# Optimization experiments

Hardware: AMD Instinct MI355X
Metric: run time of the kernel (lower is better)

## Reference

```python
import jax, jax.numpy as jnp
import numpy as np

D_MODEL = 1024
NUM_HEADS = 16
D_K = D_MODEL // NUM_HEADS


def setup_inputs() -> dict:
    key = jax.random.key(0)
    ks = jax.random.split(key, 8)
    B, S = 2, 2048
    s = 1.0 / np.sqrt(D_MODEL)
    return {
        "query": jax.random.normal(ks[0], (B, S, D_MODEL), jnp.float32),
        "key": jax.random.normal(ks[1], (B, S, D_MODEL), jnp.float32),
        "value": jax.random.normal(ks[2], (B, S, D_MODEL), jnp.float32),
        "Wq": jax.random.normal(ks[3], (D_MODEL, D_MODEL), jnp.float32) * s,
        "bq": jnp.zeros((D_MODEL,), jnp.float32),
        "Wk": jax.random.normal(ks[4], (D_MODEL, D_MODEL), jnp.float32) * s,
        "bk": jnp.zeros((D_MODEL,), jnp.float32),
        "Wv": jax.random.normal(ks[5], (D_MODEL, D_K), jnp.float32) * s,
        "bv": jnp.zeros((D_K,), jnp.float32),
        "Wo": jax.random.normal(ks[6], (D_K, D_MODEL), jnp.float32) * (1.0 / np.sqrt(D_K)),
        "bo": jnp.zeros((D_MODEL,), jnp.float32),
    }


def reference(query, key, value, Wq, bq, Wk, bk, Wv, bv, Wo, bo):
    B, S, _ = query.shape
    scale = jnp.sqrt(jnp.asarray(D_K, query.dtype))
    # Per-head Q, K: [B, H, S, d_k]
    Q = (query @ Wq + bq).reshape(B, S, NUM_HEADS, D_K).transpose(0, 2, 1, 3)
    K = (key @ Wk + bk).reshape(B, -1, NUM_HEADS, D_K).transpose(0, 2, 1, 3)
    # Shared V across heads: [B, S, d_k]
    V = value @ Wv + bv
    scores = jnp.einsum("bhqd,bhkd->bhqk", Q, K) / scale
    attn = jax.nn.softmax(scores, axis=-1)
    avg_attn = attn.mean(axis=1)            # [B, S, S] head-averaged weights
    attn_output = jnp.einsum("bqk,bkd->bqd", avg_attn, V)
    output = attn_output @ Wo + bo
    return (output, avg_attn)
```

## Files before the change

kernel.cpp:

```cpp
#include <hip/hip_runtime.h>

#define BATCH 2
#define SEQ   2048
#define DMODEL 1024
#define NHEAD 16
#define DK    64
#define MROWS (BATCH * SEQ)
#define KSPLIT 4

using bf16x8 = __attribute__((ext_vector_type(8))) short;
using f32x4  = __attribute__((ext_vector_type(4))) float;

__device__ __forceinline__ unsigned short f2bf_rne(float x) {
    unsigned u = __float_as_uint(x);
    u += 0x7FFFu + ((u >> 16) & 1u);
    return (unsigned short)(u >> 16);
}
__device__ __forceinline__ float bf2f(unsigned short h) {
    return __uint_as_float((unsigned)h << 16);
}

__device__ __forceinline__ long long qf_addr(int row, int d) {
    const int qt = row >> 4, lid = row & 15;
    const int hh = d >> 6, ch = (d >> 3) & 7, j = d & 7;
    return ((((long long)qt * NHEAD + hh) * 8 + ch) * 16 + lid) * 8 + j;
}

__global__ __launch_bounds__(256) void conv_split_kernel(
    const float* __restrict__ x, unsigned short* __restrict__ hi,
    unsigned short* __restrict__ lo)
{
    const long long i = ((long long)blockIdx.x * 256 + threadIdx.x) * 4;
    float4 v = *(const float4*)&x[i];
    ushort4 h4, l4;
    unsigned short h;
    h = f2bf_rne(v.x); h4.x = h; l4.x = f2bf_rne(v.x - bf2f(h));
    h = f2bf_rne(v.y); h4.y = h; l4.y = f2bf_rne(v.y - bf2f(h));
    h = f2bf_rne(v.z); h4.z = h; l4.z = f2bf_rne(v.z - bf2f(h));
    h = f2bf_rne(v.w); h4.w = h; l4.w = f2bf_rne(v.w - bf2f(h));
    *(ushort4*)&hi[i] = h4;
    *(ushort4*)&lo[i] = l4;
}

__global__ __launch_bounds__(256) void conv_splitT_kernel(
    const float* __restrict__ W, unsigned short* __restrict__ hiT,
    unsigned short* __restrict__ loT)
{
    const int k0 = blockIdx.y * 64;
    const int n0 = blockIdx.x * 64;
    const int tid = threadIdx.x;
    __shared__ float T[64][68];
#pragma unroll
    for (int it = 0; it < 4; ++it) {
        const int r = it * 16 + (tid >> 4);
        const int c = (tid & 15) * 4;
        float4 v = *(const float4*)&W[(long long)(k0 + r) * DMODEL + n0 + c];
        T[r][c] = v.x; T[r][c + 1] = v.y; T[r][c + 2] = v.z; T[r][c + 3] = v.w;
    }
    __syncthreads();
#pragma unroll
    for (int it = 0; it < 4; ++it) {
        const int n = it * 16 + (tid >> 4);
        const int kc = (tid & 15) * 4;
        ushort4 h4, l4;
        float v; unsigned short h;
        v = T[kc + 0][n]; h = f2bf_rne(v); h4.x = h; l4.x = f2bf_rne(v - bf2f(h));
        v = T[kc + 1][n]; h = f2bf_rne(v); h4.y = h; l4.y = f2bf_rne(v - bf2f(h));
        v = T[kc + 2][n]; h = f2bf_rne(v); h4.z = h; l4.z = f2bf_rne(v - bf2f(h));
        v = T[kc + 3][n]; h = f2bf_rne(v); h4.w = h; l4.w = f2bf_rne(v - bf2f(h));
        const long long off = (long long)(n0 + n) * DMODEL + k0 + kc;
        *(ushort4*)&hiT[off] = h4;
        *(ushort4*)&loT[off] = l4;
    }
}

#define PROW 40

__global__ __launch_bounds__(256) void proj_mfma_kernel(
    const unsigned short* __restrict__ AH, const unsigned short* __restrict__ AL,
    const unsigned short* __restrict__ BTH, const unsigned short* __restrict__ BTL,
    const float* __restrict__ bias,
    unsigned short* __restrict__ OH, unsigned short* __restrict__ OL, int fragQ)
{
    const int n0 = blockIdx.x * 128;
    const int m0 = blockIdx.y * 128;
    const int tid = threadIdx.x;
    const int w = tid >> 6, lane = tid & 63;
    const int wm = w >> 1, wn = w & 1;
    const int quad = lane >> 4, lid = lane & 15;

    __shared__ unsigned short As[2][128][PROW];
    __shared__ unsigned short Bs[2][128][PROW];

    f32x4 acc[4][4] = {};

    for (int k0 = 0; k0 < DMODEL; k0 += 32) {
        __syncthreads();
#pragma unroll
        for (int it = 0; it < 4; ++it) {
            const int cell = it * 256 + tid;
            const int half = cell >> 9;
            const int row  = (cell >> 2) & 127;
            const int c    = cell & 3;
            const unsigned short* a = half ? AL : AH;
            uint4 v = *(const uint4*)&a[(long long)(m0 + row) * DMODEL + k0 + c * 8];
            *(uint4*)&As[half][row][c * 8] = v;
            const unsigned short* b = half ? BTL : BTH;
            uint4 u = *(const uint4*)&b[(long long)(n0 + row) * DMODEL + k0 + c * 8];
            *(uint4*)&Bs[half][row][c * 8] = u;
        }
        __syncthreads();

        bf16x8 af[2][4], bf_[2][4];
#pragma unroll
        for (int mt = 0; mt < 4; ++mt) {
            const int r = wm * 64 + mt * 16 + lid;
            af[0][mt] = *(const bf16x8*)&As[0][r][quad * 8];
            af[1][mt] = *(const bf16x8*)&As[1][r][quad * 8];
        }
#pragma unroll
        for (int nt = 0; nt < 4; ++nt) {
            const int r = wn * 64 + nt * 16 + lid;
            bf_[0][nt] = *(const bf16x8*)&Bs[0][r][quad * 8];
            bf_[1][nt] = *(const bf16x8*)&Bs[1][r][quad * 8];
        }
#pragma unroll
        for (int mt = 0; mt < 4; ++mt)
#pragma unroll
            for (int nt = 0; nt < 4; ++nt) {
                acc[mt][nt] = __builtin_amdgcn_mfma_f32_16x16x32_bf16(af[0][mt], bf_[0][nt], acc[mt][nt], 0, 0, 0);
                acc[mt][nt] = __builtin_amdgcn_mfma_f32_16x16x32_bf16(af[0][mt], bf_[1][nt], acc[mt][nt], 0, 0, 0);
                acc[mt][nt] = __builtin_amdgcn_mfma_f32_16x16x32_bf16(af[1][mt], bf_[0][nt], acc[mt][nt], 0, 0, 0);
            }
    }

    float bv[4];
#pragma unroll
    for (int nt = 0; nt < 4; ++nt)
        bv[nt] = bias[n0 + wn * 64 + nt * 16 + lid];

#pragma unroll
    for (int mt = 0; mt < 4; ++mt)
#pragma unroll
        for (int nt = 0; nt < 4; ++nt) {
            const int col = n0 + wn * 64 + nt * 16 + lid;
#pragma unroll
            for (int r = 0; r < 4; ++r) {
                const int row = m0 + wm * 64 + mt * 16 + quad * 4 + r;
                const float val = acc[mt][nt][r] + bv[nt];
                const unsigned short h = f2bf_rne(val);
                const unsigned short l = f2bf_rne(val - bf2f(h));
                if (fragQ) {
                    const long long fa = qf_addr(row, col);
                    OH[fa] = h; OL[fa] = l;
                } else {
                    const long long off = (long long)row * DMODEL + col;
                    OH[off] = h; OL[off] = l;
                }
            }
        }
}

__global__ __launch_bounds__(256) void gemm_bias_kernel(
    const float* __restrict__ A, long long sA,
    const float* __restrict__ W, long long sW,
    const float* __restrict__ bias,
    float* __restrict__ C, long long sC,
    int M, int N, int K)
{
    A += (long long)blockIdx.z * sA;
    W += (long long)blockIdx.z * sW;
    C += (long long)blockIdx.z * sC;
    const int n0 = blockIdx.x * 64;
    const int m0 = blockIdx.y * 64;

    __shared__ float As[16][68];
    __shared__ float Bs[16][68];

    const int tid = threadIdx.x;
    const int tm = (tid >> 4) << 2;
    const int tn = (tid & 15) << 2;
    const int arow = tid >> 2, ak = (tid & 3) << 2;
    const int brow = tid >> 4, bn = (tid & 15) << 2;

    float acc[4][4] = {};

    for (int k0 = 0; k0 < K; k0 += 16) {
        float4 av = *(const float4*)&A[(long long)(m0 + arow) * K + k0 + ak];
        float4 wv = *(const float4*)&W[(long long)(k0 + brow) * N + n0 + bn];
        As[ak + 0][arow] = av.x;
        As[ak + 1][arow] = av.y;
        As[ak + 2][arow] = av.z;
        As[ak + 3][arow] = av.w;
        *(float4*)&Bs[brow][bn] = wv;
        __syncthreads();
#pragma unroll
        for (int kk = 0; kk < 16; ++kk) {
            float4 a4 = *(const float4*)&As[kk][tm];
            float4 b4 = *(const float4*)&Bs[kk][tn];
            float aa[4] = {a4.x, a4.y, a4.z, a4.w};
            float bb[4] = {b4.x, b4.y, b4.z, b4.w};
#pragma unroll
            for (int i = 0; i < 4; ++i)
#pragma unroll
                for (int j = 0; j < 4; ++j)
                    acc[i][j] = fmaf(aa[i], bb[j], acc[i][j]);
        }
        __syncthreads();
    }

    float4 bv = make_float4(0.f, 0.f, 0.f, 0.f);
    if (bias) bv = *(const float4*)&bias[n0 + tn];
#pragma unroll
    for (int i = 0; i < 4; ++i) {
        float4 o = make_float4(acc[i][0] + bv.x, acc[i][1] + bv.y,
                               acc[i][2] + bv.z, acc[i][3] + bv.w);
        *(float4*)&C[(long long)(m0 + tm + i) * N + n0 + tn] = o;
    }
}

__global__ __launch_bounds__(256) void gemm_splitk_kernel(
    const float* __restrict__ A, long long sA,
    const float* __restrict__ W, long long sW,
    float* __restrict__ P,
    int M, int N, int K, int nsplit)
{
    const int nbatch = gridDim.z / nsplit;
    const int b = blockIdx.z / nsplit;
    const int s = blockIdx.z % nsplit;
    A += (long long)b * sA;
    W += (long long)b * sW;
    float* Pout = P + ((long long)s * nbatch + b) * M * N;

    const int n0 = blockIdx.x * 64;
    const int m0 = blockIdx.y * 64;
    const int kb = s * (K / nsplit);
    const int kl = K / nsplit;

    __shared__ float As[16][68];
    __shared__ float Bs[16][68];

    const int tid = threadIdx.x;
    const int tm = (tid >> 4) << 2;
    const int tn = (tid & 15) << 2;
    const int arow = tid >> 2, ak = (tid & 3) << 2;
    const int brow = tid >> 4, bn = (tid & 15) << 2;

    float acc[4][4] = {};

    for (int k0 = 0; k0 < kl; k0 += 16) {
        float4 av = *(const float4*)&A[(long long)(m0 + arow) * K + kb + k0 + ak];
        float4 wv = *(const float4*)&W[(long long)(kb + k0 + brow) * N + n0 + bn];
        As[ak + 0][arow] = av.x;
        As[ak + 1][arow] = av.y;
        As[ak + 2][arow] = av.z;
        As[ak + 3][arow] = av.w;
        *(float4*)&Bs[brow][bn] = wv;
        __syncthreads();
#pragma unroll
        for (int kk = 0; kk < 16; ++kk) {
            float4 a4 = *(const float4*)&As[kk][tm];
            float4 b4 = *(const float4*)&Bs[kk][tn];
            float aa[4] = {a4.x, a4.y, a4.z, a4.w};
            float bb[4] = {b4.x, b4.y, b4.z, b4.w};
#pragma unroll
            for (int i = 0; i < 4; ++i)
#pragma unroll
                for (int j = 0; j < 4; ++j)
                    acc[i][j] = fmaf(aa[i], bb[j], acc[i][j]);
        }
        __syncthreads();
    }

#pragma unroll
    for (int i = 0; i < 4; ++i) {
        float4 o = make_float4(acc[i][0], acc[i][1], acc[i][2], acc[i][3]);
        *(float4*)&Pout[(long long)(m0 + tm + i) * N + n0 + tn] = o;
    }
}

__global__ __launch_bounds__(256) void reduce_bias_kernel(
    const float* __restrict__ P, const float* __restrict__ bias,
    float* __restrict__ C, long long stride, int nsplit, int N)
{
    const long long i = ((long long)blockIdx.x * 256 + threadIdx.x) * 4;
    float4 s = *(const float4*)&P[i];
    for (int k = 1; k < nsplit; ++k) {
        float4 v = *(const float4*)&P[(long long)k * stride + i];
        s.x += v.x; s.y += v.y; s.z += v.z; s.w += v.w;
    }
    if (bias) {
        const int n = (int)(i % N);
        float4 b4 = *(const float4*)&bias[n];
        s.x += b4.x; s.y += b4.y; s.z += b4.z; s.w += b4.w;
    }
    *(float4*)&C[i] = s;
}

#define KROW 80
#define KHALF (128 * KROW)

__device__ __forceinline__ void stage_K(
    const unsigned short* __restrict__ Khi, const unsigned short* __restrict__ Klo,
    unsigned short* Ks, long long grow0, int h, int tid)
{
#pragma unroll
    for (int it = 0; it < 8; ++it) {
        const int cell = it * 256 + tid;
        const int half = cell >> 10;
        const int row  = (cell >> 3) & 127;
        const int ch   = cell & 7;
        const unsigned short* src = half ? Klo : Khi;
        uint4 v = *(const uint4*)&src[(grow0 + row) * DMODEL + h * 64 + ch * 8];
        *(uint4*)&Ks[half * KHALF + row * KROW + ch * 8] = v;
    }
}

__device__ __forceinline__ f32x4 mfma3(bf16x8 ah, bf16x8 al, bf16x8 bh, bf16x8 bl, f32x4 s) {
    s = __builtin_amdgcn_mfma_f32_16x16x32_bf16(ah, bh, s, 0, 0, 0);
    s = __builtin_amdgcn_mfma_f32_16x16x32_bf16(ah, bl, s, 0, 0, 0);
    s = __builtin_amdgcn_mfma_f32_16x16x32_bf16(al, bh, s, 0, 0, 0);
    return s;
}

__global__ __launch_bounds__(256) void attn_stats_kernel(
    const unsigned short* __restrict__ QfH, const unsigned short* __restrict__ QfL,
    const unsigned short* __restrict__ Khi, const unsigned short* __restrict__ Klo,
    float* __restrict__ lsum)
{
    const int q0 = blockIdx.x * 128;
    const int h  = blockIdx.y;
    const int b  = blockIdx.z >> 2;
    const int kbase = (blockIdx.z & 3) * (SEQ / KSPLIT);
    const int tid = threadIdx.x;
    const int w = tid >> 6, lane = tid & 63;
    const int quad = lane >> 4, lid = lane & 15;

    __shared__ unsigned short Ks[2 * KHALF];

    bf16x8 ah[2][2], al[2][2];
#pragma unroll
    for (int mt = 0; mt < 2; ++mt) {
        const long long qt = (long long)(b * SEQ + q0) / 16 + w * 2 + mt;
#pragma unroll
        for (int ks = 0; ks < 2; ++ks) {
            const long long fa = (((qt * NHEAD + h) * 8 + (quad + 4 * ks)) * 16 + lid) * 8;
            ah[mt][ks] = *(const bf16x8*)&QfH[fa];
            al[mt][ks] = *(const bf16x8*)&QfL[fa];
        }
    }

    float ls[2][4] = {};
    const long long grow0 = (long long)b * SEQ + kbase;

    for (int kc = 0; kc < SEQ / KSPLIT; kc += 128) {
        __syncthreads();
        stage_K(Khi, Klo, Ks, grow0 + kc, h, tid);
        __syncthreads();

#pragma unroll
        for (int kt = 0; kt < 8; ++kt) {
            bf16x8 bh[2], bl[2];
#pragma unroll
            for (int ks = 0; ks < 2; ++ks) {
                const int o = (kt * 16 + lid) * KROW + (quad + 4 * ks) * 8;
                bh[ks] = *(const bf16x8*)&Ks[o];
                bl[ks] = *(const bf16x8*)&Ks[KHALF + o];
            }
#pragma unroll
            for (int mt = 0; mt < 2; ++mt) {
                f32x4 s = {0.f, 0.f, 0.f, 0.f};
#pragma unroll
                for (int ks = 0; ks < 2; ++ks)
                    s = mfma3(ah[mt][ks], al[mt][ks], bh[ks], bl[ks], s);
#pragma unroll
                for (int r = 0; r < 4; ++r)
                    ls[mt][r] += __expf(s[r] * 0.125f);
            }
        }
    }

#pragma unroll
    for (int off = 1; off < 16; off <<= 1)
#pragma unroll
        for (int mt = 0; mt < 2; ++mt)
#pragma unroll
            for (int r = 0; r < 4; ++r)
                ls[mt][r] += __shfl_xor(ls[mt][r], off);

    if (lid == 0) {
        const long long base = ((long long)(b * NHEAD + h)) * SEQ + q0 + w * 32 + quad * 4;
#pragma unroll
        for (int mt = 0; mt < 2; ++mt)
#pragma unroll
            for (int r = 0; r < 4; ++r)
                atomicAdd(&lsum[base + mt * 16 + r], ls[mt][r]);
    }
}

__global__ __launch_bounds__(256) void recip_kernel(float* __restrict__ p) {
    const int i = blockIdx.x * 256 + threadIdx.x;
    p[i] = 0.0625f / p[i];
}

__global__ __launch_bounds__(256) void attn_avg_kernel(
    const unsigned short* __restrict__ QfH, const unsigned short* __restrict__ QfL,
    const unsigned short* __restrict__ Khi, const unsigned short* __restrict__ Klo,
    const float* __restrict__ cIn, float* __restrict__ avg)
{
    const int q0 = blockIdx.x * 128;
    const int k0 = blockIdx.y * 128;
    const int b  = blockIdx.z;
    const int tid = threadIdx.x;
    const int w = tid >> 6, lane = tid & 63;
    const int quad = lane >> 4, lid = lane & 15;

    __shared__ unsigned short Ks[2 * KHALF];

    f32x4 acc[2][8] = {};
    const long long grow0 = (long long)b * SEQ + k0;

    for (int h = 0; h < NHEAD; ++h) {
        __syncthreads();
        stage_K(Khi, Klo, Ks, grow0, h, tid);

        bf16x8 ah[2][2], al[2][2];
        float c_[2][4];
#pragma unroll
        for (int mt = 0; mt < 2; ++mt) {
            const long long qt = (long long)(b * SEQ + q0) / 16 + w * 2 + mt;
#pragma unroll
            for (int ks = 0; ks < 2; ++ks) {
                const long long fa = (((qt * NHEAD + h) * 8 + (quad + 4 * ks)) * 16 + lid) * 8;
                ah[mt][ks] = *(const bf16x8*)&QfH[fa];
                al[mt][ks] = *(const bf16x8*)&QfL[fa];
            }
            const long long cb = ((long long)(b * NHEAD + h)) * SEQ + q0 + w * 32 + mt * 16 + quad * 4;
#pragma unroll
            for (int r = 0; r < 4; ++r)
                c_[mt][r] = cIn[cb + r];
        }
        __syncthreads();

#pragma unroll
        for (int kt = 0; kt < 8; ++kt) {
            bf16x8 bh[2], bl[2];
#pragma unroll
            for (int ks = 0; ks < 2; ++ks) {
                const int o = (kt * 16 + lid) * KROW + (quad + 4 * ks) * 8;
                bh[ks] = *(const bf16x8*)&Ks[o];
                bl[ks] = *(const bf16x8*)&Ks[KHALF + o];
            }
#pragma unroll
            for (int mt = 0; mt < 2; ++mt) {
                f32x4 s = {0.f, 0.f, 0.f, 0.f};
#pragma unroll
                for (int ks = 0; ks < 2; ++ks)
                    s = mfma3(ah[mt][ks], al[mt][ks], bh[ks], bl[ks], s);
#pragma unroll
                for (int r = 0; r < 4; ++r)
                    acc[mt][kt][r] = fmaf(__expf(s[r] * 0.125f), c_[mt][r], acc[mt][kt][r]);
            }
        }
    }

#pragma unroll
    for (int mt = 0; mt < 2; ++mt)
#pragma unroll
        for (int kt = 0; kt < 8; ++kt)
#pragma unroll
            for (int r = 0; r < 4; ++r) {
                const int q = q0 + w * 32 + mt * 16 + quad * 4 + r;
                avg[((long long)(b * SEQ + q)) * SEQ + k0 + kt * 16 + lid] = acc[mt][kt][r];
            }
}

extern "C" void kernel_launch(void* const* d_in, const int* in_sizes, int n_in,
                              void* d_out, int out_size, void* d_ws, size_t ws_size,
                              hipStream_t stream)
{
    const float* query = (const float*)d_in[0];
    const float* key   = (const float*)d_in[1];
    const float* value = (const float*)d_in[2];
    const float* Wq    = (const float*)d_in[3];
    const float* bq    = (const float*)d_in[4];
    const float* Wk    = (const float*)d_in[5];
    const float* bk    = (const float*)d_in[6];
    const float* Wv    = (const float*)d_in[7];
    const float* bv    = (const float*)d_in[8];
    const float* Wo    = (const float*)d_in[9];
    const float* bo    = (const float*)d_in[10];

    float* out = (float*)d_out;
    float* avg = out + (long long)BATCH * SEQ * DMODEL;

    const long long QKN = (long long)MROWS * DMODEL;
    unsigned short* QfH = (unsigned short*)d_ws;
    unsigned short* QfL = QfH + QKN;
    unsigned short* Khi = QfL + QKN;
    unsigned short* Klo = Khi + QKN;
    unsigned short* AspH = Klo + QKN;
    unsigned short* AspL = AspH + QKN;
    unsigned short* WTh  = AspL + QKN;
    unsigned short* WTl  = WTh + (long long)DMODEL * DMODEL;
    float* Vb   = (float*)(WTl + (long long)DMODEL * DMODEL);
    float* lBuf = Vb + (long long)MROWS * DK;
    float* ao   = lBuf + (long long)BATCH * NHEAD * SEQ;

    float* Pv  = (float*)AspH;
    float* Pav = (float*)QfH;

    dim3 blk(256);
    hipMemsetAsync(lBuf, 0, (size_t)BATCH * NHEAD * SEQ * sizeof(float), stream);

    const int convGrid = (int)(QKN / (256 * 4));
    dim3 tGrid(DMODEL / 64, DMODEL / 64);
    dim3 pGrid(DMODEL / 128, MROWS / 128);

    conv_split_kernel<<<convGrid, blk, 0, stream>>>(query, AspH, AspL);
    conv_splitT_kernel<<<tGrid, blk, 0, stream>>>(Wq, WTh, WTl);
    proj_mfma_kernel<<<pGrid, blk, 0, stream>>>(AspH, AspL, WTh, WTl, bq, QfH, QfL, 1);

    conv_split_kernel<<<convGrid, blk, 0, stream>>>(key, AspH, AspL);
    conv_splitT_kernel<<<tGrid, blk, 0, stream>>>(Wk, WTh, WTl);
    proj_mfma_kernel<<<pGrid, blk, 0, stream>>>(AspH, AspL, WTh, WTl, bk, Khi, Klo, 0);

    gemm_splitk_kernel<<<dim3(DK / 64, MROWS / 64, 16), blk, 0, stream>>>(
        value, 0, Wv, 0, Pv, MROWS, DK, DMODEL, 16);
    reduce_bias_kernel<<<dim3((int)((long long)MROWS * DK / 1024)), blk, 0, stream>>>(
        Pv, bv, Vb, (long long)MROWS * DK, 16, DK);

    attn_stats_kernel<<<dim3(SEQ / 128, NHEAD, BATCH * KSPLIT), blk, 0, stream>>>(
        QfH, QfL, Khi, Klo, lBuf);
    recip_kernel<<<dim3(BATCH * NHEAD * SEQ / 256), blk, 0, stream>>>(lBuf);

    attn_avg_kernel<<<dim3(SEQ / 128, SEQ / 128, BATCH), blk, 0, stream>>>(
        QfH, QfL, Khi, Klo, lBuf, avg);

    gemm_splitk_kernel<<<dim3(DK / 64, SEQ / 64, BATCH * 32), blk, 0, stream>>>(
        avg, (long long)SEQ * SEQ, Vb, (long long)SEQ * DK, Pav, SEQ, DK, SEQ, 32);
    reduce_bias_kernel<<<dim3((int)((long long)MROWS * DK / 1024)), blk, 0, stream>>>(
        Pav, nullptr, ao, (long long)MROWS * DK, 32, DK);

    gemm_bias_kernel<<<dim3(DMODEL / 64, MROWS / 64, 1), blk, 0, stream>>>(
        ao, 0, Wo, 0, bo, out, 0, MROWS, DMODEL, DK);
}
```

Measured before the change: 436.3 us.

## Double-buffer K tiles with direct global-to-LDS loads and XOR swizzle

Replaces the register-staged K tile copy into padded shared memory with direct global_load_lds transfers into a double-buffered, XOR-swizzled LDS layout, in both the stats and averaging attention kernels. The next tile (next key chunk or next head) is issued before computing on the current one, so load latency overlaps with the MFMA work and one barrier per iteration is removed. This doubles LDS use per block, which may lower occupancy. Correctness relies on the async LDS writes having completed by the trailing __syncthreads, and there is no explicit vmcnt wait.

```diff
diff --git a/kernel.cpp b/kernel.cpp
--- a/kernel.cpp
+++ b/kernel.cpp
@@ -297,22 +297,26 @@
     *(float4*)&C[i] = s;
 }
 
-#define KROW 80
-#define KHALF (128 * KROW)
-
-__device__ __forceinline__ void stage_K(
+#define HALF_USH 8192
+#define TILE_USH 16384
+
+__device__ __forceinline__ void stage_issue(
     const unsigned short* __restrict__ Khi, const unsigned short* __restrict__ Klo,
-    unsigned short* Ks, long long grow0, int h, int tid)
-{
+    unsigned short* KsBuf, long long grow0, int h, int w, int lane)
+{
+    const int rsub = lane >> 3;
+    const int slot = (lane & 7) ^ rsub;
 #pragma unroll
     for (int it = 0; it < 8; ++it) {
-        const int cell = it * 256 + tid;
-        const int half = cell >> 10;
-        const int row  = (cell >> 3) & 127;
-        const int ch   = cell & 7;
+        const int c = it * 4 + w;
+        const int half = c >> 4;
+        const int row  = (c & 15) * 8 + rsub;
         const unsigned short* src = half ? Klo : Khi;
-        uint4 v = *(const uint4*)&src[(grow0 + row) * DMODEL + h * 64 + ch * 8];
-        *(uint4*)&Ks[half * KHALF + row * KROW + ch * 8] = v;
+        const unsigned short* g = &src[(grow0 + row) * DMODEL + h * 64 + slot * 8];
+        __builtin_amdgcn_global_load_lds(
+            (const __attribute__((address_space(1))) unsigned int*)g,
+            (__attribute__((address_space(3))) unsigned int*)(KsBuf + c * 512),
+            16, 0, 0);
     }
 }
 
@@ -336,7 +340,7 @@
     const int w = tid >> 6, lane = tid & 63;
     const int quad = lane >> 4, lid = lane & 15;
 
-    __shared__ unsigned short Ks[2 * KHALF];
+    __shared__ unsigned short Ks[2 * TILE_USH];
 
     bf16x8 ah[2][2], al[2][2];
 #pragma unroll
@@ -353,19 +357,26 @@
     float ls[2][4] = {};
     const long long grow0 = (long long)b * SEQ + kbase;
 
+    stage_issue(Khi, Klo, Ks, grow0, h, w, lane);
+    __syncthreads();
+
     for (int kc = 0; kc < SEQ / KSPLIT; kc += 128) {
-        __syncthreads();
-        stage_K(Khi, Klo, Ks, grow0 + kc, h, tid);
-        __syncthreads();
+        const int buf = (kc >> 7) & 1;
+        if (kc + 128 < SEQ / KSPLIT)
+            stage_issue(Khi, Klo, Ks + (buf ^ 1) * TILE_USH,
+                        grow0 + kc + 128, h, w, lane);
+        const unsigned short* Kc = Ks + buf * TILE_USH;
 
 #pragma unroll
         for (int kt = 0; kt < 8; ++kt) {
+            const int rr = kt * 16 + lid;
+            const int sw = rr & 7;
             bf16x8 bh[2], bl[2];
 #pragma unroll
             for (int ks = 0; ks < 2; ++ks) {
-                const int o = (kt * 16 + lid) * KROW + (quad + 4 * ks) * 8;
-                bh[ks] = *(const bf16x8*)&Ks[o];
-                bl[ks] = *(const bf16x8*)&Ks[KHALF + o];
+                const int o = rr * 64 + (((quad + 4 * ks) ^ sw) * 8);
+                bh[ks] = *(const bf16x8*)&Kc[o];
+                bl[ks] = *(const bf16x8*)&Kc[HALF_USH + o];
             }
 #pragma unroll
             for (int mt = 0; mt < 2; ++mt) {
@@ -378,6 +389,7 @@
                     ls[mt][r] += __expf(s[r] * 0.125f);
             }
         }
+        __syncthreads();
     }
 
 #pragma unroll
@@ -415,15 +427,15 @@
     const int w = tid >> 6, lane = tid & 63;
     const int quad = lane >> 4, lid = lane & 15;
 
-    __shared__ unsigned short Ks[2 * KHALF];
+    __shared__ unsigned short Ks[2 * TILE_USH];
 
     f32x4 acc[2][8] = {};
     const long long grow0 = (long long)b * SEQ + k0;
 
+    stage_issue(Khi, Klo, Ks, grow0, 0, w, lane);
+    __syncthreads();
+
     for (int h = 0; h < NHEAD; ++h) {
-        __syncthreads();
-        stage_K(Khi, Klo, Ks, grow0, h, tid);
-
         bf16x8 ah[2][2], al[2][2];
         float c_[2][4];
 #pragma unroll
@@ -440,16 +452,23 @@
             for (int r = 0; r < 4; ++r)
                 c_[mt][r] = cIn[cb + r];
         }
-        __syncthreads();
+
+        const int buf = h & 1;
+        if (h + 1 < NHEAD)
+            stage_issue(Khi, Klo, Ks + (buf ^ 1) * TILE_USH,
+                        grow0, h + 1, w, lane);
+        const unsigned short* Kc = Ks + buf * TILE_USH;
 
 #pragma unroll
         for (int kt = 0; kt < 8; ++kt) {
+            const int rr = kt * 16 + lid;
+            const int sw = rr & 7;
             bf16x8 bh[2], bl[2];
 #pragma unroll
             for (int ks = 0; ks < 2; ++ks) {
-                const int o = (kt * 16 + lid) * KROW + (quad + 4 * ks) * 8;
-                bh[ks] = *(const bf16x8*)&Ks[o];
-                bl[ks] = *(const bf16x8*)&Ks[KHALF + o];
+                const int o = rr * 64 + (((quad + 4 * ks) ^ sw) * 8);
+                bh[ks] = *(const bf16x8*)&Kc[o];
+                bl[ks] = *(const bf16x8*)&Kc[HALF_USH + o];
             }
 #pragma unroll
             for (int mt = 0; mt < 2; ++mt) {
@@ -462,6 +481,7 @@
                     acc[mt][kt][r] = fmaf(__expf(s[r] * 0.125f), c_[mt][r], acc[mt][kt][r]);
             }
         }
+        __syncthreads();
     }
 
 #pragma unroll
```

After: 430.4 us. Within noise of the previous version (-1.3%).
